# Kernel tuning notes

Hardware: AMD Instinct MI355X
Metric: run time of the kernel (lower is better)

Reference implementation:

```python
import jax, jax.numpy as jnp
import numpy as np

D_MODEL = 2048
D_INNER = 2048
D_XB = 512
N_HEADS = 32
HEADDIM = 64   # P
DSTATE = 64    # N
N_KV = D_XB // DSTATE          # 8 kv heads
REP = N_HEADS // N_KV
D_FF = 8192
DCONV = 4
EPS = 1e-5
B, L = 1, 2048


def _rmsnorm(x, w, eps=EPS):
    return x * jax.lax.rsqrt(jnp.mean(x * x, axis=-1, keepdims=True) + eps) * w


def _silu(x):
    return x * jax.nn.sigmoid(x)


def _causal_dwconv(x, w, b):
    # x: (B,L,C), depthwise causal conv, kernel DCONV
    xp = jnp.pad(x, ((0, 0), (DCONV - 1, 0), (0, 0)))
    y = b
    for k in range(DCONV):  # small fixed kernel loop
        y = y + xp[:, k:k + x.shape[1], :] * w[:, k]
    return y


def setup_inputs() -> dict:
    key = jax.random.key(0)
    ks = jax.random.split(key, 10)
    s = 0.02
    d_proj = 2 * D_INNER + 2 * D_XB + N_HEADS  # z, x, B, C, dt
    conv_ch = 2 * D_XB + D_INNER               # conv over concat(x, B, C)
    return {
        "hidden_states": jax.random.normal(ks[0], (B, L, D_MODEL), jnp.float32),
        "in_proj_w": jax.random.normal(ks[1], (d_proj, D_MODEL), jnp.float32) * s,
        "conv_w": jax.random.normal(ks[2], (conv_ch, DCONV), jnp.float32) * s,
        "conv_b": jnp.zeros((conv_ch,), jnp.float32),
        "dt_bias": jax.random.normal(ks[3], (N_HEADS,), jnp.float32) * s,
        "A_log": jnp.log(jnp.arange(1, N_HEADS + 1, dtype=jnp.float32)),
        "D": jnp.ones((N_HEADS,), jnp.float32),
        "ssm_norm_w": jnp.ones((D_INNER,), jnp.float32),
        "out_proj_w": jax.random.normal(ks[4], (D_MODEL, D_INNER), jnp.float32) * s,
        "input_ln_w": jnp.ones((D_MODEL,), jnp.float32),
        "post_ln_w": jnp.ones((D_MODEL,), jnp.float32),
        "gate_w": jax.random.normal(ks[5], (D_FF, D_MODEL), jnp.float32) * s,
        "up_w": jax.random.normal(ks[6], (D_FF, D_MODEL), jnp.float32) * s,
        "down_w": jax.random.normal(ks[7], (D_MODEL, D_FF), jnp.float32) * s,
    }


def _mamba2(hs, in_proj_w, conv_w, conv_b, dt_bias, A_log, D, ssm_norm_w, out_proj_w):
    b, l, _ = hs.shape
    zxbcdt = hs @ in_proj_w.T
    z, x, Bm, Cm, dt = jnp.split(
        zxbcdt, [D_INNER, D_INNER + D_XB, D_INNER + 2 * D_XB, 2 * D_INNER + 2 * D_XB], axis=-1)
    # causal depthwise conv + silu over concat(x, B, C)
    xBC = _silu(_causal_dwconv(jnp.concatenate([x, Bm, Cm], axis=-1), conv_w, conv_b))
    x, Bm, Cm = jnp.split(xBC, [D_XB, 2 * D_XB], axis=-1)
    # heads (GQA: repeat x and B from N_KV to N_HEADS)
    x = jnp.repeat(x.reshape(b, l, N_KV, HEADDIM), REP, axis=2)      # (b,l,H,P)
    Bm = jnp.repeat(Bm.reshape(b, l, N_KV, DSTATE), REP, axis=2)     # (b,l,H,N)
    Cm = Cm.reshape(b, l, N_HEADS, DSTATE)                            # (b,l,H,N)
    dt = jax.nn.softplus(dt + dt_bias)                                # (b,l,H)
    dA = jnp.exp(dt * (-jnp.exp(A_log)))                              # (b,l,H)
    # selective scan over time
    xs = (jnp.moveaxis(dA, 1, 0), jnp.moveaxis(dt, 1, 0),
          jnp.moveaxis(x, 1, 0), jnp.moveaxis(Bm, 1, 0), jnp.moveaxis(Cm, 1, 0))
    h0 = jnp.zeros((b, N_HEADS, HEADDIM, DSTATE), hs.dtype)

    def step(h, t):
        dA_t, dt_t, x_t, B_t, C_t = t
        h = h * dA_t[:, :, None, None] + jnp.einsum('bh,bhp,bhn->bhpn', dt_t, x_t, B_t)
        y = jnp.einsum('bhpn,bhn->bhp', h, C_t)
        return h, y

    _, ys = jax.lax.scan(step, h0, xs)            # (l,b,H,P)
    y = jnp.moveaxis(ys, 0, 1) + D[None, None, :, None] * x
    y = y.reshape(b, l, D_INNER)
    y = _rmsnorm(y * _silu(z), ssm_norm_w)        # gated RMSNorm
    return y @ out_proj_w.T


def reference(hidden_states, in_proj_w, conv_w, conv_b, dt_bias, A_log, D,
              ssm_norm_w, out_proj_w, input_ln_w, post_ln_w, gate_w, up_w, down_w):
    residual = hidden_states
    h = _rmsnorm(hidden_states, input_ln_w)
    h = residual + _mamba2(h, in_proj_w, conv_w, conv_b, dt_bias, A_log, D,
                           ssm_norm_w, out_proj_w)
    residual = h
    h = _rmsnorm(h, post_ln_w)
    h = (_silu(h @ gate_w.T) * (h @ up_w.T)) @ down_w.T
    return residual + h
```

## Files before the change

### kernel.cpp

```cpp
#include <hip/hip_runtime.h>

typedef unsigned short u16;
typedef unsigned int u32;
typedef float f32x4 __attribute__((ext_vector_type(4)));
typedef __bf16 bf16x8 __attribute__((ext_vector_type(8)));
typedef unsigned short u16x8 __attribute__((ext_vector_type(8)));

#define L_SEQ 2048
#define DMODEL 2048
#define DINNER 2048
#define DXB 512
#define NHEADS 32
#define DPROJ 5152
#define DPROJ_PAD 5376
#define CONVCH 3072
#define DFF 8192
#define NCHUNK 32
#define CHUNK 64

__device__ __forceinline__ float bf2f(u16 u) {
  union { unsigned int i; float f; } v; v.i = ((unsigned int)u) << 16; return v.f;
}
__device__ __forceinline__ u16 f2bf(float f) {
  union { float f; unsigned int i; } v; v.f = f;
  unsigned int u = v.i;
  u += 0x7FFFu + ((u >> 16) & 1u);
  return (u16)(u >> 16);
}
__device__ __forceinline__ float siluf(float x) { return x / (1.f + __expf(-x)); }

#define GL16(gsrc, ldst) \
  __builtin_amdgcn_global_load_lds((const __attribute__((address_space(1))) u32*)(gsrc), \
                                   (__attribute__((address_space(3))) u32*)(ldst), 16, 0, 0)
#define SBAR() __builtin_amdgcn_s_barrier()
#define WAIT_VM4() asm volatile("s_waitcnt vmcnt(4)" ::: "memory")
#define WAIT_VM0() asm volatile("s_waitcnt vmcnt(0)" ::: "memory")

__global__ __launch_bounds__(256) void cvt_k(
    const float* __restrict__ s, u16* __restrict__ d, int n8)
{
  const int i = blockIdx.x * 256 + threadIdx.x;
  if (i >= n8) return;
  f32x4 a = *(const f32x4*)(s + (size_t)i * 8);
  f32x4 b = *(const f32x4*)(s + (size_t)i * 8 + 4);
  u16x8 o;
#pragma unroll
  for (int j = 0; j < 4; ++j) { o[j] = f2bf(a[j]); o[j + 4] = f2bf(b[j]); }
  *(u16x8*)(d + (size_t)i * 8) = o;
}

__global__ __launch_bounds__(256) void cvt_pad_k(
    const float* __restrict__ s, u16* __restrict__ d)
{
  const int i = blockIdx.x * 256 + threadIdx.x;
  const int row = (i * 8) >> 11;
  u16x8 o;
  if (row < DPROJ) {
    f32x4 a = *(const f32x4*)(s + (size_t)i * 8);
    f32x4 b = *(const f32x4*)(s + (size_t)i * 8 + 4);
#pragma unroll
    for (int j = 0; j < 4; ++j) { o[j] = f2bf(a[j]); o[j + 4] = f2bf(b[j]); }
  } else {
#pragma unroll
    for (int j = 0; j < 8; ++j) o[j] = 0;
  }
  *(u16x8*)(d + (size_t)i * 8) = o;
}

template<int MH, int NH>
__device__ __forceinline__ void mfma16(f32x4 (&acc)[8][4], const bf16x8 (&af)[4][2],
                                       const bf16x8 (&bfq)[2][2][2]) {
#pragma unroll
  for (int s = 0; s < 2; ++s)
#pragma unroll
    for (int m = 0; m < 4; ++m)
#pragma unroll
      for (int n = 0; n < 2; ++n)
        acc[MH * 4 + m][NH * 2 + n] = __builtin_amdgcn_mfma_f32_16x16x32_bf16(
            af[m][s], bfq[NH][n][s], acc[MH * 4 + m][NH * 2 + n], 0, 0, 0);
}

template<int EPI, int SPLIT>
__global__ __launch_bounds__(512, 2) void gemm8(
    const u16* __restrict__ A, const u16* __restrict__ W,
    void* __restrict__ Cptr, const u16* __restrict__ gateB,
    const int N, const int K, const int gx)
{
  __shared__ u16 sm[65536];
  const int tid = threadIdx.x;
  const int wid = tid >> 6, ln = tid & 63;
  const int wm = wid >> 2, wn = wid & 3;

  const int nwg = gridDim.x;
  int wg = (int)blockIdx.x;
  wg = (wg & 7) * (nwg >> 3) + (wg >> 3);
  const int tilesPerZ = gx << 3;
  const int bz = wg / tilesPerZ;
  const int rem = wg - bz * tilesPerZ;
  const int bx = rem >> 3;
  const int by = rem & 7;
  const int m0 = by << 8, n0 = bx << 8;
  const int NT = (K >> 6) / SPLIT;
  const int ktB = bz * NT;

  f32x4 acc[8][4];
#pragma unroll
  for (int i = 0; i < 8; ++i)
#pragma unroll
    for (int j = 0; j < 4; ++j) acc[i][j] = f32x4{0.f, 0.f, 0.f, 0.f};

  const int l8r = ln >> 3;
  const int schunk = (ln & 7) ^ l8r;
  const int lr16 = ln & 15;
  const int q4 = ln >> 4;
  const int swz = ln & 7;
  const int c0 = ((q4 ^ swz) << 3);

  auto stageA = [&](int buf, int kt, int h) {
#pragma unroll
    for (int g = 0; g < 2; ++g) {
      const int rr = (wid << 3) + l8r;
      const size_t grow = (size_t)(m0 + (g << 7) + (h << 6) + rr);
      const u16* src = A + grow * K + (size_t)((ktB + kt) << 6) + (schunk << 3);
      u16* dst = &sm[(buf << 15) + (((h << 7) + (g << 6) + (wid << 3)) << 6)];
      GL16(src, dst);
    }
  };
  auto stageB = [&](int buf, int kt, int h) {
#pragma unroll
    for (int g = 0; g < 2; ++g) {
      const int v = (g << 6) + (wid << 3) + l8r;
      const int grow = n0 + ((v >> 5) << 6) + (h << 5) + (v & 31);
      const u16* src = W + (size_t)grow * K + (size_t)((ktB + kt) << 6) + (schunk << 3);
      u16* dst = &sm[(buf << 15) + 16384 + (((h << 7) + (g << 6) + (wid << 3)) << 6)];
      GL16(src, dst);
    }
  };

  bf16x8 af[4][2], bfq[2][2][2];
  auto loadA = [&](int buf, int mh) {
#pragma unroll
    for (int m = 0; m < 4; ++m) {
      const int lrA = (mh << 7) + (wm << 6) + (m << 4) + lr16;
      const u16* p = &sm[(buf << 15) + (lrA << 6)];
      af[m][0] = *(const bf16x8*)(p + c0);
      af[m][1] = *(const bf16x8*)(p + (c0 ^ 32));
    }
  };
  auto loadB = [&](int buf, int nh) {
#pragma unroll
    for (int n = 0; n < 2; ++n) {
      const int lrB = (nh << 7) + (wn << 5) + (n << 4) + lr16;
      const u16* p = &sm[(buf << 15) + 16384 + (lrB << 6)];
      bfq[nh][n][0] = *(const bf16x8*)(p + c0);
      bfq[nh][n][1] = *(const bf16x8*)(p + (c0 ^ 32));
    }
  };

  stageA(0, 0, 0); stageA(0, 0, 1); stageB(0, 0, 0); stageB(0, 0, 1);
  stageA(1, 1, 0); stageB(1, 1, 1);
  WAIT_VM4();
  SBAR();

  for (int kt = 0; kt < NT; kt += 2) {
    const bool s2 = (kt + 2) < NT, s3 = (kt + 3) < NT;
    loadA(0, 0); loadB(0, 0);
    stageA(1, kt + 1, 1);
    __builtin_amdgcn_s_setprio(1); mfma16<0, 0>(acc, af, bfq); __builtin_amdgcn_s_setprio(0);
    SBAR();
    loadB(0, 1);
    stageB(1, kt + 1, 0);
    __builtin_amdgcn_s_setprio(1); mfma16<0, 1>(acc, af, bfq); __builtin_amdgcn_s_setprio(0);
    SBAR();
    loadA(0, 1);
    if (s2) stageA(0, kt + 2, 0);
    __builtin_amdgcn_s_setprio(1); mfma16<1, 1>(acc, af, bfq); __builtin_amdgcn_s_setprio(0);
    SBAR();
    if (s2) stageB(0, kt + 2, 1);
    __builtin_amdgcn_s_setprio(1); mfma16<1, 0>(acc, af, bfq); __builtin_amdgcn_s_setprio(0);
    if (s2) { WAIT_VM4(); } else { WAIT_VM0(); }
    SBAR();
    loadA(1, 0); loadB(1, 0);
    if (s2) stageA(0, kt + 2, 1);
    __builtin_amdgcn_s_setprio(1); mfma16<0, 0>(acc, af, bfq); __builtin_amdgcn_s_setprio(0);
    SBAR();
    loadB(1, 1);
    if (s2) stageB(0, kt + 2, 0);
    __builtin_amdgcn_s_setprio(1); mfma16<0, 1>(acc, af, bfq); __builtin_amdgcn_s_setprio(0);
    SBAR();
    loadA(1, 1);
    if (s3) stageA(1, kt + 3, 0);
    __builtin_amdgcn_s_setprio(1); mfma16<1, 1>(acc, af, bfq); __builtin_amdgcn_s_setprio(0);
    SBAR();
    if (s3) stageB(1, kt + 3, 1);
    __builtin_amdgcn_s_setprio(1); mfma16<1, 0>(acc, af, bfq); __builtin_amdgcn_s_setprio(0);
    if (s2) { if (s3) { WAIT_VM4(); } else { WAIT_VM0(); } }
    SBAR();
  }

  const int crow0 = m0 + (wm << 7) + (q4 << 2);
  const int ccol0 = n0 + (wn << 6) + lr16;
#pragma unroll
  for (int M = 0; M < 8; ++M) {
#pragma unroll
    for (int n = 0; n < 4; ++n) {
      const int col = ccol0 + (n << 4);
      if (col < N) {
#pragma unroll
        for (int j = 0; j < 4; ++j) {
          const size_t idx = (size_t)(crow0 + (M << 4) + j) * N + col;
          if (EPI == 0) {
            ((u16*)Cptr)[idx] = f2bf(acc[M][n][j]);
          } else if (EPI == 2) {
            float* P = (float*)Cptr + (size_t)bz * ((size_t)L_SEQ * N);
            P[idx] = acc[M][n][j];
          } else {
            ((u16*)Cptr)[idx] = f2bf(siluf(bf2f(gateB[idx])) * acc[M][n][j]);
          }
        }
      }
    }
  }
}

__global__ __launch_bounds__(256) void rmsnorm_k(
    const float* __restrict__ in, const float* __restrict__ w, u16* __restrict__ out)
{
  const int row = blockIdx.x, tid = threadIdx.x;
  const float* r = in + (size_t)row * DMODEL + tid * 8;
  f32x4 v0 = *(const f32x4*)r;
  f32x4 v1 = *(const f32x4*)(r + 4);
  float ss = v0[0]*v0[0] + v0[1]*v0[1] + v0[2]*v0[2] + v0[3]*v0[3]
           + v1[0]*v1[0] + v1[1]*v1[1] + v1[2]*v1[2] + v1[3]*v1[3];
#pragma unroll
  for (int off = 1; off < 64; off <<= 1) ss += __shfl_xor(ss, off);
  __shared__ float part[4];
  if ((tid & 63) == 0) part[tid >> 6] = ss;
  __syncthreads();
  const float tot = part[0] + part[1] + part[2] + part[3];
  const float scale = rsqrtf(tot * (1.f / DMODEL) + 1e-5f);
  f32x4 w0 = *(const f32x4*)(w + tid * 8);
  f32x4 w1 = *(const f32x4*)(w + tid * 8 + 4);
  u16x8 o;
#pragma unroll
  for (int j = 0; j < 4; ++j) {
    o[j]     = f2bf(v0[j] * scale * w0[j]);
    o[j + 4] = f2bf(v1[j] * scale * w1[j]);
  }
  *(u16x8*)(out + (size_t)row * DMODEL + tid * 8) = o;
}

__global__ __launch_bounds__(256) void red4_rms_k(
    const float* __restrict__ P, const float* __restrict__ resid,
    float* __restrict__ hres, const float* __restrict__ w, u16* __restrict__ h2)
{
  const int row = blockIdx.x, tid = threadIdx.x;
  const size_t base = (size_t)row * DMODEL + tid * 8;
  const size_t stride = (size_t)L_SEQ * DMODEL;
  f32x4 v0 = *(const f32x4*)(resid + base);
  f32x4 v1 = *(const f32x4*)(resid + base + 4);
#pragma unroll
  for (int p = 0; p < 4; ++p) {
    v0 += *(const f32x4*)(P + p * stride + base);
    v1 += *(const f32x4*)(P + p * stride + base + 4);
  }
  *(f32x4*)(hres + base) = v0;
  *(f32x4*)(hres + base + 4) = v1;
  float ss = v0[0]*v0[0] + v0[1]*v0[1] + v0[2]*v0[2] + v0[3]*v0[3]
           + v1[0]*v1[0] + v1[1]*v1[1] + v1[2]*v1[2] + v1[3]*v1[3];
#pragma unroll
  for (int off = 1; off < 64; off <<= 1) ss += __shfl_xor(ss, off);
  __shared__ float part[4];
  if ((tid & 63) == 0) part[tid >> 6] = ss;
  __syncthreads();
  const float tot = part[0] + part[1] + part[2] + part[3];
  const float scale = rsqrtf(tot * (1.f / DMODEL) + 1e-5f);
  f32x4 w0 = *(const f32x4*)(w + tid * 8);
  f32x4 w1 = *(const f32x4*)(w + tid * 8 + 4);
  u16x8 o;
#pragma unroll
  for (int j = 0; j < 4; ++j) {
    o[j]     = f2bf(v0[j] * scale * w0[j]);
    o[j + 4] = f2bf(v1[j] * scale * w1[j]);
  }
  *(u16x8*)(h2 + base) = o;
}

__global__ __launch_bounds__(256) void red4_add_k(
    const float* __restrict__ P, const float* __restrict__ resid, float* __restrict__ out)
{
  const size_t base = ((size_t)blockIdx.x * 256 + threadIdx.x) * 8;
  const size_t stride = (size_t)L_SEQ * DMODEL;
  f32x4 v0 = *(const f32x4*)(resid + base);
  f32x4 v1 = *(const f32x4*)(resid + base + 4);
#pragma unroll
  for (int p = 0; p < 4; ++p) {
    v0 += *(const f32x4*)(P + p * stride + base);
    v1 += *(const f32x4*)(P + p * stride + base + 4);
  }
  *(f32x4*)(out + base) = v0;
  *(f32x4*)(out + base + 4) = v1;
}

__global__ __launch_bounds__(256) void gated_rms_k(
    const float* __restrict__ y, const u16* __restrict__ zx,
    const float* __restrict__ w, u16* __restrict__ out)
{
  const int row = blockIdx.x, tid = threadIdx.x;
  const float* yr = y + (size_t)row * DINNER + tid * 8;
  f32x4 y0 = *(const f32x4*)yr;
  f32x4 y1 = *(const f32x4*)(yr + 4);
  u16x8 zv = *(const u16x8*)(zx + (size_t)row * DPROJ + tid * 8);
  float val[8];
#pragma unroll
  for (int j = 0; j < 4; ++j) {
    val[j]     = y0[j] * siluf(bf2f(zv[j]));
    val[j + 4] = y1[j] * siluf(bf2f(zv[j + 4]));
  }
  float ss = 0.f;
#pragma unroll
  for (int j = 0; j < 8; ++j) ss += val[j] * val[j];
#pragma unroll
  for (int off = 1; off < 64; off <<= 1) ss += __shfl_xor(ss, off);
  __shared__ float part[4];
  if ((tid & 63) == 0) part[tid >> 6] = ss;
  __syncthreads();
  const float tot = part[0] + part[1] + part[2] + part[3];
  const float scale = rsqrtf(tot * (1.f / DINNER) + 1e-5f);
  u16x8 o;
#pragma unroll
  for (int j = 0; j < 8; ++j) o[j] = f2bf(val[j] * scale * w[tid * 8 + j]);
  *(u16x8*)(out + (size_t)row * DINNER + tid * 8) = o;
}

__global__ __launch_bounds__(256) void convdt_k(
    const u16* __restrict__ zx, const float* __restrict__ w,
    const float* __restrict__ b, u16* __restrict__ xbc,
    const float* __restrict__ dt_bias, const float* __restrict__ A_log,
    float* __restrict__ dtv, float* __restrict__ dAv)
{
  if (blockIdx.x < 3072) {
    const int flat = blockIdx.x * 256 + threadIdx.x;
    const int t = flat / 384;
    const int c8 = (flat % 384) * 8;
    float acc[8];
    f32x4 b0 = *(const f32x4*)(b + c8);
    f32x4 b1 = *(const f32x4*)(b + c8 + 4);
#pragma unroll
    for (int j = 0; j < 4; ++j) { acc[j] = b0[j]; acc[j + 4] = b1[j]; }
    f32x4 wr[8];
#pragma unroll
    for (int j = 0; j < 8; ++j) wr[j] = *(const f32x4*)(w + (size_t)(c8 + j) * 4);
#pragma unroll
    for (int k = 0; k < 4; ++k) {
      const int tt = t - 3 + k;
      if (tt >= 0) {
        u16x8 xv = *(const u16x8*)(zx + (size_t)tt * DPROJ + DINNER + c8);
#pragma unroll
        for (int j = 0; j < 8; ++j) acc[j] += bf2f(xv[j]) * wr[j][k];
      }
    }
    u16x8 o;
#pragma unroll
    for (int j = 0; j < 8; ++j) o[j] = f2bf(siluf(acc[j]));
    *(u16x8*)(xbc + (size_t)t * CONVCH + c8) = o;
  } else {
    const int flat = (blockIdx.x - 3072) * 256 + threadIdx.x;
    const int t = flat >> 5, h = flat & 31;
    const float x = bf2f(zx[(size_t)t * DPROJ + (DPROJ - NHEADS) + h]) + dt_bias[h];
    const float sp = (x > 20.f) ? x : log1pf(expf(x));
    const float a = expf(A_log[h]);
    dtv[flat] = sp;
    dAv[flat] = expf(-a * sp);
  }
}

__device__ __forceinline__ void stage16(float* dst, const u16* src) {
  u16x8 a = *(const u16x8*)src;
  u16x8 b = *(const u16x8*)(src + 8);
#pragma unroll
  for (int j = 0; j < 8; ++j) { dst[j] = bf2f(a[j]); dst[8 + j] = bf2f(b[j]); }
}

__global__ __launch_bounds__(256) void scan_a(
    const u16* __restrict__ xbc, const float* __restrict__ dtv,
    const float* __restrict__ dAv, const float* __restrict__ Dvec,
    float* __restrict__ y, float* __restrict__ S,
    float* __restrict__ gam, float* __restrict__ cum)
{
  __shared__ float xs[64][64], Bs[64][64], Cs[64][64];
  __shared__ float dts[64], dAs[64];
  const int c = blockIdx.x, h = blockIdx.y, kv = h >> 2;
  const int tid = threadIdx.x;
  const int t0 = c * CHUNK;
  {
    const int r = tid >> 2, cq = (tid & 3) * 16;
    const u16* base = xbc + (size_t)(t0 + r) * CONVCH;
    stage16(&xs[r][cq], base + kv * 64 + cq);
    stage16(&Bs[r][cq], base + DXB + kv * 64 + cq);
    stage16(&Cs[r][cq], base + 2 * DXB + h * 64 + cq);
    if (tid < 64) {
      dts[tid] = dtv[(size_t)(t0 + tid) * NHEADS + h];
      dAs[tid] = dAv[(size_t)(t0 + tid) * NHEADS + h];
    }
  }
  __syncthreads();
  const int p = tid >> 2, q = tid & 3;
  float hreg[16];
#pragma unroll
  for (int i = 0; i < 16; ++i) hreg[i] = 0.f;
  float cumv = 1.f;
  const float Dh = Dvec[h];
  for (int t = 0; t < CHUNK; ++t) {
    const float dtt = dts[t], dat = dAs[t];
    const float xv = xs[t][p];
    const float u = dtt * xv;
    float a0 = 0.f, a1 = 0.f, a2 = 0.f, a3 = 0.f;
#pragma unroll
    for (int i4 = 0; i4 < 4; ++i4) {
      f32x4 b4 = *(const f32x4*)&Bs[t][q * 16 + i4 * 4];
      f32x4 c4 = *(const f32x4*)&Cs[t][q * 16 + i4 * 4];
#pragma unroll
      for (int j = 0; j < 4; ++j) {
        const int i = i4 * 4 + j;
        hreg[i] = hreg[i] * dat + u * b4[j];
        if (i4 == 0) a0 += hreg[i] * c4[j];
        else if (i4 == 1) a1 += hreg[i] * c4[j];
        else if (i4 == 2) a2 += hreg[i] * c4[j];
        else a3 += hreg[i] * c4[j];
      }
    }
    float accv = (a0 + a1) + (a2 + a3);
    accv += __shfl_xor(accv, 1);
    accv += __shfl_xor(accv, 2);
    cumv *= dat;
    if (q == 0) y[(size_t)(t0 + t) * DINNER + h * 64 + p] = accv + Dh * xv;
    if (tid == 0) cum[(size_t)(t0 + t) * NHEADS + h] = cumv;
  }
  float* Sp = S + ((size_t)(c * NHEADS + h) << 12) + tid * 16;
#pragma unroll
  for (int i4 = 0; i4 < 4; ++i4)
    *(f32x4*)(Sp + i4 * 4) = f32x4{hreg[i4*4], hreg[i4*4+1], hreg[i4*4+2], hreg[i4*4+3]};
  if (tid == 0) gam[c * NHEADS + h] = cumv;
}

__global__ __launch_bounds__(256) void scan_b(
    const float* __restrict__ S, const float* __restrict__ gam, float* __restrict__ H)
{
  const int h = blockIdx.x, tid = threadIdx.x;
  float hr[16];
#pragma unroll
  for (int i = 0; i < 16; ++i) hr[i] = 0.f;
  for (int c = 0; c < NCHUNK; ++c) {
    const size_t base = ((size_t)(c * NHEADS + h) << 12) + tid * 16;
#pragma unroll
    for (int i4 = 0; i4 < 4; ++i4)
      *(f32x4*)(H + base + i4 * 4) = f32x4{hr[i4*4], hr[i4*4+1], hr[i4*4+2], hr[i4*4+3]};
    const float g = gam[c * NHEADS + h];
#pragma unroll
    for (int i4 = 0; i4 < 4; ++i4) {
      f32x4 s = *(const f32x4*)(S + base + i4 * 4);
#pragma unroll
      for (int j = 0; j < 4; ++j) hr[i4 * 4 + j] = g * hr[i4 * 4 + j] + s[j];
    }
  }
}

__global__ __launch_bounds__(256) void scan_c(
    const u16* __restrict__ xbc, const float* __restrict__ cum,
    const float* __restrict__ H, float* __restrict__ y)
{
  __shared__ float Cs[64][64];
  __shared__ float cums[64];
  const int c = blockIdx.x, h = blockIdx.y, tid = threadIdx.x;
  const int t0 = c * CHUNK;
  {
    const int r = tid >> 2, cq = (tid & 3) * 16;
    stage16(&Cs[r][cq], xbc + (size_t)(t0 + r) * CONVCH + 2 * DXB + h * 64 + cq);
    if (tid < 64) cums[tid] = cum[(size_t)(t0 + tid) * NHEADS + h];
  }
  const int p = tid >> 2, q = tid & 3;
  float hr[16];
  const size_t base = ((size_t)(c * NHEADS + h) << 12) + tid * 16;
#pragma unroll
  for (int i4 = 0; i4 < 4; ++i4) {
    f32x4 v = *(const f32x4*)(H + base + i4 * 4);
#pragma unroll
    for (int j = 0; j < 4; ++j) hr[i4 * 4 + j] = v[j];
  }
  __syncthreads();
  for (int t = 0; t < CHUNK; ++t) {
    float accv = 0.f;
#pragma unroll
    for (int i4 = 0; i4 < 4; ++i4) {
      f32x4 c4 = *(const f32x4*)&Cs[t][q * 16 + i4 * 4];
#pragma unroll
      for (int j = 0; j < 4; ++j) accv += hr[i4 * 4 + j] * c4[j];
    }
    accv += __shfl_xor(accv, 1);
    accv += __shfl_xor(accv, 2);
    if (q == 0) {
      const size_t idx = (size_t)(t0 + t) * DINNER + h * 64 + p;
      y[idx] += cums[t] * accv;
    }
  }
}

extern "C" void kernel_launch(void* const* d_in, const int* in_sizes, int n_in,
                              void* d_out, int out_size, void* d_ws, size_t ws_size,
                              hipStream_t stream) {
  const float* hs         = (const float*)d_in[0];
  const float* in_proj_w  = (const float*)d_in[1];
  const float* conv_w     = (const float*)d_in[2];
  const float* conv_b     = (const float*)d_in[3];
  const float* dt_bias    = (const float*)d_in[4];
  const float* A_log      = (const float*)d_in[5];
  const float* Dv         = (const float*)d_in[6];
  const float* ssm_w      = (const float*)d_in[7];
  const float* out_proj_w = (const float*)d_in[8];
  const float* in_ln_w    = (const float*)d_in[9];
  const float* post_ln_w  = (const float*)d_in[10];
  const float* gate_w     = (const float*)d_in[11];
  const float* up_w       = (const float*)d_in[12];
  const float* down_w     = (const float*)d_in[13];
  float* out = (float*)d_out;

  char* ws = (char*)d_ws;
  size_t off = 0;
  auto alloc = [&](size_t bytes) -> void* {
    void* p = ws + off;
    off = (off + bytes + 255) & ~(size_t)255;
    return p;
  };
  u16* wip = (u16*)alloc((size_t)DPROJ_PAD * DMODEL * 2);
  u16* wop = (u16*)alloc((size_t)DMODEL * DINNER * 2);
  u16* wg  = (u16*)alloc((size_t)DFF    * DMODEL * 2);
  u16* wu  = (u16*)alloc((size_t)DFF    * DMODEL * 2);
  u16* wd  = (u16*)alloc((size_t)DMODEL * DFF    * 2);
  u16*   zx  = (u16*)  alloc((size_t)L_SEQ * DPROJ * 2);
  u16*   xbc = (u16*)  alloc((size_t)L_SEQ * CONVCH * 2);
  float* Sv  = (float*)alloc((size_t)NCHUNK * NHEADS * 4096 * 4);
  float* Hv  = (float*)alloc((size_t)NCHUNK * NHEADS * 4096 * 4);
  float* pK  = (float*)zx;
  float* dtv = (float*)alloc((size_t)L_SEQ * NHEADS * 4);
  float* dAv = (float*)alloc((size_t)L_SEQ * NHEADS * 4);
  float* cum = (float*)alloc((size_t)L_SEQ * NHEADS * 4);
  float* gam = (float*)alloc((size_t)NCHUNK * NHEADS * 4);
  float* yv  = (float*)alloc((size_t)L_SEQ * DINNER * 4);
  float* hres= (float*)alloc((size_t)L_SEQ * DMODEL * 4);
  u16*  gateb= (u16*)  alloc((size_t)L_SEQ * DFF * 2);
  u16*  hslot= (u16*)  alloc((size_t)L_SEQ * DMODEL * 2);
  (void)ws_size; (void)in_sizes; (void)n_in; (void)out_size;

  cvt_pad_k<<<(DPROJ_PAD * DMODEL / 8) / 256, 256, 0, stream>>>(in_proj_w, wip);
  cvt_k<<<DMODEL * DINNER / 8 / 256, 256, 0, stream>>>(out_proj_w, wop, DMODEL * DINNER / 8);
  cvt_k<<<DFF * DMODEL / 8 / 256, 256, 0, stream>>>(gate_w, wg, DFF * DMODEL / 8);
  cvt_k<<<DFF * DMODEL / 8 / 256, 256, 0, stream>>>(up_w, wu, DFF * DMODEL / 8);
  cvt_k<<<DMODEL * DFF / 8 / 256, 256, 0, stream>>>(down_w, wd, DMODEL * DFF / 8);

  rmsnorm_k<<<L_SEQ, 256, 0, stream>>>(hs, in_ln_w, hslot);
  gemm8<0, 1><<<21 * 8, 512, 0, stream>>>(hslot, wip, zx, nullptr, DPROJ, DMODEL, 21);
  convdt_k<<<3072 + 256, 256, 0, stream>>>(zx, conv_w, conv_b, xbc, dt_bias, A_log, dtv, dAv);
  scan_a<<<dim3(NCHUNK, NHEADS), 256, 0, stream>>>(xbc, dtv, dAv, Dv, yv, Sv, gam, cum);
  scan_b<<<NHEADS, 256, 0, stream>>>(Sv, gam, Hv);
  scan_c<<<dim3(NCHUNK, NHEADS), 256, 0, stream>>>(xbc, cum, Hv, yv);
  gated_rms_k<<<L_SEQ, 256, 0, stream>>>(yv, zx, ssm_w, hslot);
  gemm8<2, 4><<<8 * 8 * 4, 512, 0, stream>>>(hslot, wop, pK, nullptr, DMODEL, DINNER, 8);
  red4_rms_k<<<L_SEQ, 256, 0, stream>>>(pK, hs, hres, post_ln_w, hslot);
  gemm8<0, 1><<<32 * 8, 512, 0, stream>>>(hslot, wg, gateb, nullptr, DFF, DMODEL, 32);
  gemm8<3, 1><<<32 * 8, 512, 0, stream>>>(hslot, wu, gateb, gateb, DFF, DMODEL, 32);
  gemm8<2, 4><<<8 * 8 * 4, 512, 0, stream>>>(gateb, wd, pK, nullptr, DMODEL, DFF, 8);
  red4_add_k<<<(L_SEQ * DMODEL / 8) / 256, 256, 0, stream>>>(pK, hres, out);
}
```

Before: 523.4 us.

## Parallelize inter-chunk state scan across elements and merge GEMM pipeline phases

The inter-chunk state recurrence kernel now launches one thread per state element (512 blocks) instead of 32 blocks that each handle 16 elements per thread. This spreads its memory traffic across many more CUs and should cut the latency of a tiny, underfilled launch. Separately, the GEMM main loop fuses pairs of MFMA sub-phases, halving the number of block barriers per k-tile. The cost is more LDS fragment loads held live at once, which raises register pressure and gives less fine-grained interleaving of staging with compute.

```diff
diff --git a/kernel.cpp b/kernel.cpp
--- a/kernel.cpp
+++ b/kernel.cpp
@@ -164,36 +164,30 @@
 
   for (int kt = 0; kt < NT; kt += 2) {
     const bool s2 = (kt + 2) < NT, s3 = (kt + 3) < NT;
-    loadA(0, 0); loadB(0, 0);
-    stageA(1, kt + 1, 1);
-    __builtin_amdgcn_s_setprio(1); mfma16<0, 0>(acc, af, bfq); __builtin_amdgcn_s_setprio(0);
-    SBAR();
-    loadB(0, 1);
-    stageB(1, kt + 1, 0);
-    __builtin_amdgcn_s_setprio(1); mfma16<0, 1>(acc, af, bfq); __builtin_amdgcn_s_setprio(0);
+    loadA(0, 0); loadB(0, 0); loadB(0, 1);
+    stageA(1, kt + 1, 1); stageB(1, kt + 1, 0);
+    __builtin_amdgcn_s_setprio(1);
+    mfma16<0, 0>(acc, af, bfq); mfma16<0, 1>(acc, af, bfq);
+    __builtin_amdgcn_s_setprio(0);
     SBAR();
     loadA(0, 1);
-    if (s2) stageA(0, kt + 2, 0);
-    __builtin_amdgcn_s_setprio(1); mfma16<1, 1>(acc, af, bfq); __builtin_amdgcn_s_setprio(0);
-    SBAR();
-    if (s2) stageB(0, kt + 2, 1);
-    __builtin_amdgcn_s_setprio(1); mfma16<1, 0>(acc, af, bfq); __builtin_amdgcn_s_setprio(0);
+    if (s2) { stageA(0, kt + 2, 0); stageB(0, kt + 2, 1); }
+    __builtin_amdgcn_s_setprio(1);
+    mfma16<1, 1>(acc, af, bfq); mfma16<1, 0>(acc, af, bfq);
+    __builtin_amdgcn_s_setprio(0);
     if (s2) { WAIT_VM4(); } else { WAIT_VM0(); }
     SBAR();
-    loadA(1, 0); loadB(1, 0);
-    if (s2) stageA(0, kt + 2, 1);
-    __builtin_amdgcn_s_setprio(1); mfma16<0, 0>(acc, af, bfq); __builtin_amdgcn_s_setprio(0);
-    SBAR();
-    loadB(1, 1);
-    if (s2) stageB(0, kt + 2, 0);
-    __builtin_amdgcn_s_setprio(1); mfma16<0, 1>(acc, af, bfq); __builtin_amdgcn_s_setprio(0);
+    loadA(1, 0); loadB(1, 0); loadB(1, 1);
+    if (s2) { stageA(0, kt + 2, 1); stageB(0, kt + 2, 0); }
+    __builtin_amdgcn_s_setprio(1);
+    mfma16<0, 0>(acc, af, bfq); mfma16<0, 1>(acc, af, bfq);
+    __builtin_amdgcn_s_setprio(0);
     SBAR();
     loadA(1, 1);
-    if (s3) stageA(1, kt + 3, 0);
-    __builtin_amdgcn_s_setprio(1); mfma16<1, 1>(acc, af, bfq); __builtin_amdgcn_s_setprio(0);
-    SBAR();
-    if (s3) stageB(1, kt + 3, 1);
-    __builtin_amdgcn_s_setprio(1); mfma16<1, 0>(acc, af, bfq); __builtin_amdgcn_s_setprio(0);
+    if (s3) { stageA(1, kt + 3, 0); stageB(1, kt + 3, 1); }
+    __builtin_amdgcn_s_setprio(1);
+    mfma16<1, 1>(acc, af, bfq); mfma16<1, 0>(acc, af, bfq);
+    __builtin_amdgcn_s_setprio(0);
     if (s2) { if (s3) { WAIT_VM4(); } else { WAIT_VM0(); } }
     SBAR();
   }
@@ -447,22 +441,14 @@
 __global__ __launch_bounds__(256) void scan_b(
     const float* __restrict__ S, const float* __restrict__ gam, float* __restrict__ H)
 {
-  const int h = blockIdx.x, tid = threadIdx.x;
-  float hr[16];
-#pragma unroll
-  for (int i = 0; i < 16; ++i) hr[i] = 0.f;
+  const int g = blockIdx.x * 256 + threadIdx.x;
+  const int h = g >> 12;
+  const int e = g & 4095;
+  float hr = 0.f;
   for (int c = 0; c < NCHUNK; ++c) {
-    const size_t base = ((size_t)(c * NHEADS + h) << 12) + tid * 16;
-#pragma unroll
-    for (int i4 = 0; i4 < 4; ++i4)
-      *(f32x4*)(H + base + i4 * 4) = f32x4{hr[i4*4], hr[i4*4+1], hr[i4*4+2], hr[i4*4+3]};
-    const float g = gam[c * NHEADS + h];
-#pragma unroll
-    for (int i4 = 0; i4 < 4; ++i4) {
-      f32x4 s = *(const f32x4*)(S + base + i4 * 4);
-#pragma unroll
-      for (int j = 0; j < 4; ++j) hr[i4 * 4 + j] = g * hr[i4 * 4 + j] + s[j];
-    }
+    const size_t base = (((size_t)(c * NHEADS + h)) << 12) + e;
+    H[base] = hr;
+    hr = gam[c * NHEADS + h] * hr + S[base];
   }
 }
 
@@ -562,7 +548,7 @@
   gemm8<0, 1><<<21 * 8, 512, 0, stream>>>(hslot, wip, zx, nullptr, DPROJ, DMODEL, 21);
   convdt_k<<<3072 + 256, 256, 0, stream>>>(zx, conv_w, conv_b, xbc, dt_bias, A_log, dtv, dAv);
   scan_a<<<dim3(NCHUNK, NHEADS), 256, 0, stream>>>(xbc, dtv, dAv, Dv, yv, Sv, gam, cum);
-  scan_b<<<NHEADS, 256, 0, stream>>>(Sv, gam, Hv);
+  scan_b<<<512, 256, 0, stream>>>(Sv, gam, Hv);
   scan_c<<<dim3(NCHUNK, NHEADS), 256, 0, stream>>>(xbc, cum, Hv, yv);
   gated_rms_k<<<L_SEQ, 256, 0, stream>>>(yv, zx, ssm_w, hslot);
   gemm8<2, 4><<<8 * 8 * 4, 512, 0, stream>>>(hslot, wop, pK, nullptr, DMODEL, DINNER, 8);
```

Result: slower. 639.8 us (+22.2%).
